# Optimization experiments

Measured on AMD Instinct MI355X. Metric: run time of the kernel, lower is better.

## Reference

```python
import jax, jax.numpy as jnp
import numpy as np

NUM_HEADS = 8
AGENT_NUM = 64
THETA = 0.7


def conv2d(x, w, pad, groups=1):
    return jax.lax.conv_general_dilated(
        x, w, window_strides=(1, 1), padding=[(pad, pad), (pad, pad)],
        dimension_numbers=("NCHW", "OIHW", "NCHW"), feature_group_count=groups)


def setup_inputs() -> dict:
    key = jax.random.key(0)
    ks = jax.random.split(key, 8)
    B, C, H, W = 8, 256, 64, 64
    return {
        "x": jax.random.normal(ks[0], (B, C, H, W), jnp.float32),
        "qkv_w": jax.random.normal(ks[1], (3 * C, C, 3, 3), jnp.float32) * 0.05,
        "qkv_s": 1.0 + 0.05 * jax.random.normal(ks[2], (3 * C,), jnp.float32),
        "qkv_b": 0.05 * jax.random.normal(ks[3], (3 * C,), jnp.float32),
        "pe_w": jax.random.normal(ks[4], (C, 1, 3, 3), jnp.float32) * 0.05,
        "pe_s": 1.0 + 0.05 * jax.random.normal(ks[5], (C,), jnp.float32),
        "pe_b": 0.05 * jax.random.normal(ks[5], (C,), jnp.float32),
        "proj_w": jax.random.normal(ks[6], (C, C, 1, 1), jnp.float32) * 0.05,
        "proj_s": 1.0 + 0.05 * jax.random.normal(ks[7], (C,), jnp.float32),
        "proj_b": 0.05 * jax.random.normal(ks[7], (C,), jnp.float32),
    }


def reference(x, qkv_w, qkv_s, qkv_b, pe_w, pe_s, pe_b, proj_w, proj_s, proj_b):
    B, C, H, W = x.shape
    h, n = NUM_HEADS, AGENT_NUM
    d = C // h
    scale = d ** -0.5
    ps = int(n ** 0.5)  # pool_size = 8

    # Conv_dif (mode='hv'): normal 3x3 conv minus theta * (1x1 conv with hv-summed weights)
    out_n = conv2d(x, qkv_w, pad=1)
    dif_w = qkv_w.reshape(3 * C, C, 9)[:, :, jnp.array([1, 3, 4, 5, 7])].sum(-1)[:, :, None, None]
    out_d = conv2d(x, dif_w, pad=0)
    qkv = (out_n - THETA * out_d) * qkv_s[:, None, None] + qkv_b[:, None, None]  # folded BN

    q, k, v = jnp.split(qkv, 3, axis=1)  # each [B, C, H, W]
    qh = q.reshape(B, h, d, H * W)
    kh = k.reshape(B, h, d, H * W)
    vh = v.reshape(B, h, d, H * W)

    # adaptive avg pool q -> agent tokens (exact block mean since H,W % ps == 0)
    a = q.reshape(B, C, ps, H // ps, ps, W // ps).mean(axis=(3, 5))  # [B, C, ps, ps]
    a = a.reshape(B, C, n).transpose(0, 2, 1).reshape(B, n, h, d).transpose(0, 2, 3, 1)  # [B,h,d,n]

    # stage 1: agents attend to keys, aggregate values
    attn_k = jax.nn.softmax(jnp.einsum("bhdn,bhdN->bhnN", a, kh) * scale, axis=-1)
    attn = jnp.einsum("bhnN,bhdN->bhnd", attn_k, vh)  # [B,h,n,d]

    # stage 2: queries attend to agents
    q_attn = jax.nn.softmax(jnp.einsum("bhdN,bhdn->bhNn", qh, a) * scale, axis=-1)
    out = jnp.einsum("bhNn,bhnd->bhdN", q_attn, attn).reshape(B, C, H, W)

    # depthwise positional encoding on v (BN folded)
    pe = conv2d(v, pe_w, pad=1, groups=C) * pe_s[:, None, None] + pe_b[:, None, None]
    out = out + pe

    # 1x1 projection (BN folded, Identity act)
    out = conv2d(out, proj_w, pad=0) * proj_s[:, None, None] + proj_b[:, None, None]
    return out
```

## Files before the change

### kernel.cpp

```cpp
#include <hip/hip_runtime.h>
#include <cstdint>

typedef __attribute__((ext_vector_type(8))) short short8;
typedef __attribute__((ext_vector_type(4))) float f32x4;

#define THETA 0.7f
#define SCALE 0.17677669529663687f

__device__ __forceinline__ ushort f2b(float f) {
    uint32_t u = __float_as_uint(f);
    u += 0x7FFFu + ((u >> 16) & 1u);
    return (ushort)(u >> 16);
}
__device__ __forceinline__ float b2f(ushort b) {
    return __uint_as_float(((uint32_t)b) << 16);
}

__global__ __launch_bounds__(256) void k_pad(const float* __restrict__ x, ushort* __restrict__ xp) {
    int b = blockIdx.x >> 6, y = blockIdx.x & 63;
    int t = threadIdx.x;
    __shared__ float buf[64][65];
    for (int cc = 0; cc < 4; ++cc) {
        __syncthreads();
#pragma unroll
        for (int i = 0; i < 16; ++i) {
            int idx = i * 256 + t;
            int c = idx >> 6, xx = idx & 63;
            buf[c][xx] = x[(((size_t)b * 256 + cc * 64 + c) << 12) + (y << 6) + xx];
        }
        __syncthreads();
#pragma unroll
        for (int i = 0; i < 16; ++i) {
            int idx = i * 256 + t;
            int xx = idx >> 6, c = idx & 63;
            xp[((size_t)(b * 66 + y + 1) * 66 + (xx + 1)) * 256 + cc * 64 + c] = f2b(buf[c][xx]);
        }
    }
}

__global__ __launch_bounds__(256) void k_foldw(const float* __restrict__ w, const float* __restrict__ s,
                                               ushort* __restrict__ Wa) {
    int o = blockIdx.x, c = threadIdx.x;
    const float* wp = w + ((size_t)o * 256 + c) * 9;
    float v[9];
#pragma unroll
    for (int p = 0; p < 9; ++p) v[p] = wp[p];
    float hv = v[1] + v[3] + v[4] + v[5] + v[7];
    v[4] -= THETA * hv;
    float sc = s[o];
#pragma unroll
    for (int p = 0; p < 9; ++p)
        Wa[(size_t)o * 2304 + p * 256 + c] = f2b(v[p] * sc);
}

__global__ __launch_bounds__(256) void k_foldp(const float* __restrict__ w, const float* __restrict__ s,
                                               ushort* __restrict__ Wh, ushort* __restrict__ Wl) {
    int o = blockIdx.x, c = threadIdx.x;
    float v = w[(size_t)o * 256 + c] * s[o];
    ushort hi = f2b(v);
    Wh[(size_t)o * 256 + c] = hi;
    Wl[(size_t)o * 256 + c] = f2b(v - b2f(hi));
}

__global__ __launch_bounds__(256) void k_conv(const ushort* __restrict__ xp, const ushort* __restrict__ Wa,
                                              const float* __restrict__ qbias, float* __restrict__ qkv) {
    __shared__ ushort Al[128][40];
    __shared__ ushort Bl[128][40];
    const int t = threadIdx.x;
    const int bid0 = blockIdx.x;
    const int bid = (bid0 & 7) * 192 + (bid0 >> 3);
    const int b = bid / 192;
    const int ob = (bid % 192) >> 5;
    const int pb = bid & 31;
    const int o0 = ob << 7;
    const int lane = t & 63;
    const int w = t >> 6;
    const int rw = t >> 2;
    const int q4 = t & 3;
    const ushort* Ag0 = Wa + (size_t)(o0 + rw) * 2304 + q4 * 8;
    const ushort* Ag1 = Ag0 + (size_t)64 * 2304;
    const int y0 = pb * 2;
    const size_t xb = (size_t)b * 66 * 66 * 256;

    f32x4 acc[4][4] = {};

    const int ow2 = (w >> 1) << 6;
    const int pw2 = (w & 1) << 6;
    const int fr = lane & 15;
    const int fs = (lane >> 4) << 3;

    uint4 ra0, ra1, rb0, rb1;
    auto loadk = [&](int kn) {
        int pp = kn >> 3;
        int c0 = (kn & 7) << 5;
        int ky = pp / 3, kx = pp - ky * 3;
        ra0 = *(const uint4*)(Ag0 + kn * 32);
        ra1 = *(const uint4*)(Ag1 + kn * 32);
        const ushort* bp = xp + xb + ((size_t)((y0 + ky) * 66 + (rw + kx))) * 256 + c0 + q4 * 8;
        rb0 = *(const uint4*)bp;
        rb1 = *(const uint4*)(bp + 66 * 256);
    };
    loadk(0);
    for (int kc = 0; kc < 72; ++kc) {
        if (kc) __syncthreads();
        *(uint4*)&Al[rw][q4 * 8] = ra0;
        *(uint4*)&Al[rw + 64][q4 * 8] = ra1;
        *(uint4*)&Bl[rw][q4 * 8] = rb0;
        *(uint4*)&Bl[rw + 64][q4 * 8] = rb1;
        __syncthreads();
        if (kc < 71) loadk(kc + 1);
        short8 af[4], bf[4];
#pragma unroll
        for (int i = 0; i < 4; ++i) af[i] = *(const short8*)&Al[ow2 + i * 16 + fr][fs];
#pragma unroll
        for (int j = 0; j < 4; ++j) bf[j] = *(const short8*)&Bl[pw2 + j * 16 + fr][fs];
#pragma unroll
        for (int i = 0; i < 4; ++i)
#pragma unroll
            for (int j = 0; j < 4; ++j)
                acc[i][j] = __builtin_amdgcn_mfma_f32_16x16x32_bf16(af[i], bf[j], acc[i][j], 0, 0, 0);
    }
    const int pbase = pb * 128 + pw2 + (lane & 15);
#pragma unroll
    for (int i = 0; i < 4; ++i) {
        int o = o0 + ow2 + i * 16 + (lane >> 4) * 4;
#pragma unroll
        for (int r = 0; r < 4; ++r) {
            float bias = qbias[o + r];
            float* dst = qkv + ((size_t)b * 768 + o + r) * 4096 + pbase;
#pragma unroll
            for (int j = 0; j < 4; ++j)
                dst[j * 16] = acc[i][j][r] + bias;
        }
    }
}

__global__ __launch_bounds__(256) void k_pool(const float* __restrict__ qkv, float* __restrict__ ap) {
    const int bid = blockIdx.x;
    const int b = bid >> 8, c = bid & 255;
    const int t = threadIdx.x;
    const int y = t >> 2, xq = t & 3;
    __shared__ float lp[64][8];
    const float* qp = qkv + ((size_t)b * 768 + c) * 4096 + y * 64 + xq * 16;
    f32x4 v0 = *(const f32x4*)(qp);
    f32x4 v1 = *(const f32x4*)(qp + 4);
    f32x4 v2 = *(const f32x4*)(qp + 8);
    f32x4 v3 = *(const f32x4*)(qp + 12);
    lp[y][xq * 2] = v0.x + v0.y + v0.z + v0.w + v1.x + v1.y + v1.z + v1.w;
    lp[y][xq * 2 + 1] = v2.x + v2.y + v2.z + v2.w + v3.x + v3.y + v3.z + v3.w;
    __syncthreads();
    if (t < 64) {
        int py = t >> 3, px = t & 7;
        float s = 0;
#pragma unroll
        for (int r = 0; r < 8; ++r) s += lp[py * 8 + r][px];
        ap[((size_t)b * 256 + c) * 64 + t] = s * (1.0f / 64.0f);
    }
}

__global__ __launch_bounds__(256) void k_att1(const float* __restrict__ qkv, const float* __restrict__ ap,
                                              float* __restrict__ attn_g, float* __restrict__ s_g) {
    const int bid0 = blockIdx.x;
    const int bid = (bid0 & 7) * 64 + (bid0 >> 3);
    const int seg = bid & 7, h = (bid >> 3) & 7, b = bid >> 6;
    const int t = threadIdx.x;
    __shared__ float a_s[64][36];
    __shared__ ushort EL[256][68];
    __shared__ ushort vL[256][40];
#pragma unroll
    for (int i = 0; i < 8; ++i) {
        int idx = i * 256 + t;
        int n = idx & 63, d = idx >> 6;
        a_s[n][d] = ap[((size_t)b * 256 + h * 32 + d) * 64 + n] * SCALE;
    }
    const float* kb = qkv + ((size_t)b * 768 + 256 + h * 32) * 4096;
    const float* vb = qkv + ((size_t)b * 768 + 512 + h * 32) * 4096;
    const int n_own = t >> 2;
    const int dl = t & 3;
    float accr[8] = {0, 0, 0, 0, 0, 0, 0, 0};
    float s_acc = 0.f;
    __syncthreads();
    for (int chunk = 0; chunk < 2; ++chunk) {
        int pix = (seg * 2 + chunk) * 256 + t;
        float kr[32];
#pragma unroll
        for (int d = 0; d < 32; ++d) kr[d] = kb[(size_t)d * 4096 + pix];
#pragma unroll
        for (int i = 0; i < 4; ++i) {
            uint4 pk;
            pk.x = (uint32_t)f2b(vb[(size_t)(8 * i + 0) * 4096 + pix]) |
                   ((uint32_t)f2b(vb[(size_t)(8 * i + 1) * 4096 + pix]) << 16);
            pk.y = (uint32_t)f2b(vb[(size_t)(8 * i + 2) * 4096 + pix]) |
                   ((uint32_t)f2b(vb[(size_t)(8 * i + 3) * 4096 + pix]) << 16);
            pk.z = (uint32_t)f2b(vb[(size_t)(8 * i + 4) * 4096 + pix]) |
                   ((uint32_t)f2b(vb[(size_t)(8 * i + 5) * 4096 + pix]) << 16);
            pk.w = (uint32_t)f2b(vb[(size_t)(8 * i + 6) * 4096 + pix]) |
                   ((uint32_t)f2b(vb[(size_t)(8 * i + 7) * 4096 + pix]) << 16);
            *(uint4*)&vL[t][i * 8] = pk;
        }
#pragma unroll 1
        for (int np = 0; np < 32; ++np) {
            float l0 = 0, l1 = 0;
#pragma unroll
            for (int dq = 0; dq < 8; ++dq) {
                f32x4 a0 = *(const f32x4*)&a_s[2 * np][dq * 4];
                f32x4 a1 = *(const f32x4*)&a_s[2 * np + 1][dq * 4];
                l0 += a0.x * kr[dq * 4] + a0.y * kr[dq * 4 + 1] + a0.z * kr[dq * 4 + 2] + a0.w * kr[dq * 4 + 3];
                l1 += a1.x * kr[dq * 4] + a1.y * kr[dq * 4 + 1] + a1.z * kr[dq * 4 + 2] + a1.w * kr[dq * 4 + 3];
            }
            uint32_t e2 = (uint32_t)f2b(__expf(l0)) | ((uint32_t)f2b(__expf(l1)) << 16);
            *(uint32_t*)&EL[t][2 * np] = e2;
        }
        __syncthreads();
#pragma unroll 1
        for (int tt = 0; tt < 256; ++tt) {
            float e = b2f(EL[tt][n_own]);
            if (dl == 0) s_acc += e;
            ushort4 va = *(const ushort4*)&vL[tt][dl * 8];
            ushort4 vbx = *(const ushort4*)&vL[tt][dl * 8 + 4];
            accr[0] += e * b2f(va.x);
            accr[1] += e * b2f(va.y);
            accr[2] += e * b2f(va.z);
            accr[3] += e * b2f(va.w);
            accr[4] += e * b2f(vbx.x);
            accr[5] += e * b2f(vbx.y);
            accr[6] += e * b2f(vbx.z);
            accr[7] += e * b2f(vbx.w);
        }
        __syncthreads();
    }
#pragma unroll
    for (int i = 0; i < 8; ++i)
        atomicAdd(&attn_g[(((size_t)b * 8 + h) * 64 + n_own) * 32 + dl * 8 + i], accr[i]);
    if (dl == 0) atomicAdd(&s_g[((size_t)b * 8 + h) * 64 + n_own], s_acc);
}

__global__ __launch_bounds__(256) void k_att2(const float* __restrict__ qkv, const float* __restrict__ ap,
                                              const float* __restrict__ attn_g, const float* __restrict__ s_g,
                                              float* __restrict__ outp) {
    const int bid0 = blockIdx.x;
    const int bid = (bid0 & 7) * 128 + (bid0 >> 3);
    const int ch = bid & 15, h = (bid >> 4) & 7, b = bid >> 7;
    const int t = threadIdx.x;
    __shared__ float a2[64][36];
    __shared__ float at2[64][36];
    __shared__ float sInv[64];
#pragma unroll
    for (int i = 0; i < 8; ++i) {
        int idx = i * 256 + t;
        int n = idx & 63, d = idx >> 6;
        a2[n][d] = ap[((size_t)b * 256 + h * 32 + d) * 64 + n] * SCALE;
    }
    if (t < 64) sInv[t] = 1.0f / s_g[((size_t)b * 8 + h) * 64 + t];
    __syncthreads();
#pragma unroll
    for (int i = 0; i < 8; ++i) {
        int idx = i * 256 + t;
        int n = idx >> 5, d = idx & 31;
        at2[n][d] = attn_g[(((size_t)b * 8 + h) * 64 + n) * 32 + d] * sInv[n];
    }
    __syncthreads();
    const float* qb = qkv + ((size_t)b * 768 + h * 32) * 4096;
    int pix = ch * 256 + t;
    float qr[32];
#pragma unroll
    for (int d = 0; d < 32; ++d) qr[d] = qb[(size_t)d * 4096 + pix];
    float oacc[32] = {};
    float s = 0.f;
#pragma unroll 1
    for (int n = 0; n < 64; ++n) {
        float l = 0;
#pragma unroll
        for (int dq = 0; dq < 8; ++dq) {
            f32x4 av = *(const f32x4*)&a2[n][dq * 4];
            l += av.x * qr[dq * 4] + av.y * qr[dq * 4 + 1] + av.z * qr[dq * 4 + 2] + av.w * qr[dq * 4 + 3];
        }
        float e = __expf(l);
        s += e;
#pragma unroll
        for (int dq = 0; dq < 8; ++dq) {
            f32x4 tv = *(const f32x4*)&at2[n][dq * 4];
            oacc[dq * 4] += e * tv.x;
            oacc[dq * 4 + 1] += e * tv.y;
            oacc[dq * 4 + 2] += e * tv.z;
            oacc[dq * 4 + 3] += e * tv.w;
        }
    }
    float si = 1.0f / s;
#pragma unroll
    for (int d = 0; d < 32; ++d)
        outp[((size_t)b * 256 + h * 32 + d) * 4096 + pix] = oacc[d] * si;
}

__global__ __launch_bounds__(256) void k_pe(const float* __restrict__ qkv, const float* __restrict__ pw,
                                            const float* __restrict__ ps, const float* __restrict__ pbias,
                                            float* __restrict__ outp) {
    int gid = blockIdx.x * 256 + threadIdx.x;
    int x4 = (gid & 15) << 2;
    int y = (gid >> 4) & 63;
    int c = (gid >> 10) & 255;
    int b = gid >> 18;
    const float* vp = qkv + ((size_t)b * 768 + 512 + c) * 4096;
    const float* wp = pw + c * 9;
    float s0 = 0, s1 = 0, s2 = 0, s3 = 0;
#pragma unroll
    for (int ky = 0; ky < 3; ++ky) {
        int yy = y + ky - 1;
        if ((unsigned)yy >= 64u) continue;
        const float* rp = vp + yy * 64 + x4;
        f32x4 m = *(const f32x4*)rp;
        float lft = (x4 > 0) ? rp[-1] : 0.f;
        float rgt = (x4 < 60) ? rp[4] : 0.f;
        float w0 = wp[ky * 3], w1 = wp[ky * 3 + 1], w2 = wp[ky * 3 + 2];
        s0 += w0 * lft + w1 * m.x + w2 * m.y;
        s1 += w0 * m.x + w1 * m.y + w2 * m.z;
        s2 += w0 * m.y + w1 * m.z + w2 * m.w;
        s3 += w0 * m.z + w1 * m.w + w2 * rgt;
    }
    float sc = ps[c], bb = pbias[c];
    float* op = outp + ((size_t)b * 256 + c) * 4096 + y * 64 + x4;
    f32x4 o = *(const f32x4*)op;
    o.x += sc * s0 + bb;
    o.y += sc * s1 + bb;
    o.z += sc * s2 + bb;
    o.w += sc * s3 + bb;
    *(f32x4*)op = o;
}

__global__ __launch_bounds__(256) void k_proj(const float* __restrict__ outp, const ushort* __restrict__ Wh,
                                              const ushort* __restrict__ Wl, const float* __restrict__ pbias,
                                              float* __restrict__ out) {
    __shared__ ushort Ah[128][40];
    __shared__ ushort Alo[128][40];
    __shared__ ushort Xl[32][132];
    const int t = threadIdx.x;
    const int bid0 = blockIdx.x;
    const int bid = (bid0 & 7) * 64 + (bid0 >> 3);
    const int b = bid >> 6;
    const int ob = (bid >> 5) & 1;
    const int pb = bid & 31;
    const int o0 = ob << 7;
    const int p0 = pb << 7;
    const int lane = t & 63;
    const int w = t >> 6;
    const int rw = t >> 2, q4 = t & 3;
    const int cl = t >> 3, pg = t & 7;
    const int ow2 = (w >> 1) << 6;
    const int pw2 = (w & 1) << 6;
    const int fr = lane & 15;
    const int fs = (lane >> 4) << 3;

    f32x4 acc[4][4] = {};
    uint4 rah0, rah1, ral0, ral1;
    f32x4 rx[4];
    auto loadk = [&](int kc) {
        const size_t awoff = (size_t)(o0 + rw) * 256 + kc * 32 + q4 * 8;
        rah0 = *(const uint4*)(Wh + awoff);
        rah1 = *(const uint4*)(Wh + awoff + (size_t)64 * 256);
        ral0 = *(const uint4*)(Wl + awoff);
        ral1 = *(const uint4*)(Wl + awoff + (size_t)64 * 256);
        const float* xsrc = outp + ((size_t)b * 256 + kc * 32 + cl) * 4096 + p0 + pg * 16;
#pragma unroll
        for (int m = 0; m < 4; ++m) rx[m] = *(const f32x4*)(xsrc + m * 4);
    };
    loadk(0);
    for (int kc = 0; kc < 8; ++kc) {
        if (kc) __syncthreads();
        *(uint4*)&Ah[rw][q4 * 8] = rah0;
        *(uint4*)&Ah[rw + 64][q4 * 8] = rah1;
        *(uint4*)&Alo[rw][q4 * 8] = ral0;
        *(uint4*)&Alo[rw + 64][q4 * 8] = ral1;
#pragma unroll
        for (int m = 0; m < 4; ++m) {
            ushort4 u;
            u.x = f2b(rx[m].x);
            u.y = f2b(rx[m].y);
            u.z = f2b(rx[m].z);
            u.w = f2b(rx[m].w);
            *(ushort4*)&Xl[cl][pg * 16 + m * 4] = u;
        }
        __syncthreads();
        if (kc < 7) loadk(kc + 1);
        short8 ah[4], al[4], bf[4];
#pragma unroll
        for (int i = 0; i < 4; ++i) {
            ah[i] = *(const short8*)&Ah[ow2 + i * 16 + fr][fs];
            al[i] = *(const short8*)&Alo[ow2 + i * 16 + fr][fs];
        }
#pragma unroll
        for (int j = 0; j < 4; ++j) {
            int pl = pw2 + j * 16 + fr;
#pragma unroll
            for (int kk = 0; kk < 8; ++kk) bf[j][kk] = (short)Xl[fs + kk][pl];
        }
#pragma unroll
        for (int i = 0; i < 4; ++i)
#pragma unroll
            for (int j = 0; j < 4; ++j) {
                acc[i][j] = __builtin_amdgcn_mfma_f32_16x16x32_bf16(ah[i], bf[j], acc[i][j], 0, 0, 0);
                acc[i][j] = __builtin_amdgcn_mfma_f32_16x16x32_bf16(al[i], bf[j], acc[i][j], 0, 0, 0);
            }
    }
    const int pbase = p0 + pw2 + (lane & 15);
#pragma unroll
    for (int i = 0; i < 4; ++i) {
        int o = o0 + ow2 + i * 16 + (lane >> 4) * 4;
#pragma unroll
        for (int r = 0; r < 4; ++r) {
            float bias = pbias[o + r];
            float* dst = out + ((size_t)b * 256 + o + r) * 4096 + pbase;
#pragma unroll
            for (int j = 0; j < 4; ++j)
                dst[j * 16] = acc[i][j][r] + bias;
        }
    }
}

extern "C" void kernel_launch(void* const* d_in, const int* in_sizes, int n_in,
                              void* d_out, int out_size, void* d_ws, size_t ws_size,
                              hipStream_t stream) {
    const float* x = (const float*)d_in[0];
    const float* qkv_w = (const float*)d_in[1];
    const float* qkv_s = (const float*)d_in[2];
    const float* qkv_b = (const float*)d_in[3];
    const float* pe_w = (const float*)d_in[4];
    const float* pe_s = (const float*)d_in[5];
    const float* pe_b = (const float*)d_in[6];
    const float* proj_w = (const float*)d_in[7];
    const float* proj_s = (const float*)d_in[8];
    const float* proj_b = (const float*)d_in[9];
    float* out = (float*)d_out;

    char* ws = (char*)d_ws;
    ushort* xp = (ushort*)(ws);
    ushort* Wa = (ushort*)(ws + 17842176);
    float* qkv = (float*)(ws + 21381120);
    float* apool = (float*)(ws + 122044416);
    float* attn_g = (float*)(ws + 122568704);
    float* s_g = (float*)(ws + 123092992);
    float* outp = (float*)(ws + 123109376);
    ushort* Wh = (ushort*)(ws + 156663808);
    ushort* Wl = (ushort*)(ws + 156794880);

    hipMemsetAsync(xp, 0, 17842176, stream);
    hipMemsetAsync(attn_g, 0, 524288 + 16384, stream);
    k_pad<<<512, 256, 0, stream>>>(x, xp);
    k_foldw<<<768, 256, 0, stream>>>(qkv_w, qkv_s, Wa);
    k_foldp<<<256, 256, 0, stream>>>(proj_w, proj_s, Wh, Wl);
    k_conv<<<1536, 256, 0, stream>>>(xp, Wa, qkv_b, qkv);
    k_pool<<<2048, 256, 0, stream>>>(qkv, apool);
    k_att1<<<512, 256, 0, stream>>>(qkv, apool, attn_g, s_g);
    k_att2<<<1024, 256, 0, stream>>>(qkv, apool, attn_g, s_g, outp);
    k_pe<<<8192, 256, 0, stream>>>(qkv, pe_w, pe_s, pe_b, outp);
    k_proj<<<512, 256, 0, stream>>>(outp, Wh, Wl, proj_b, out);
}
```

Baseline: 451.8 us.

## Store qkv and attention output in bf16 and fuse positional conv into att2

```diff
diff --git a/kernel.cpp b/kernel.cpp
--- a/kernel.cpp
+++ b/kernel.cpp
@@ -63,7 +63,7 @@
 }
 
 __global__ __launch_bounds__(256) void k_conv(const ushort* __restrict__ xp, const ushort* __restrict__ Wa,
-                                              const float* __restrict__ qbias, float* __restrict__ qkv) {
+                                              const float* __restrict__ qbias, ushort* __restrict__ qkv) {
     __shared__ ushort Al[128][40];
     __shared__ ushort Bl[128][40];
     const int t = threadIdx.x;
@@ -127,27 +127,30 @@
 #pragma unroll
         for (int r = 0; r < 4; ++r) {
             float bias = qbias[o + r];
-            float* dst = qkv + ((size_t)b * 768 + o + r) * 4096 + pbase;
+            ushort* dst = qkv + ((size_t)b * 768 + o + r) * 4096 + pbase;
 #pragma unroll
             for (int j = 0; j < 4; ++j)
-                dst[j * 16] = acc[i][j][r] + bias;
-        }
-    }
-}
-
-__global__ __launch_bounds__(256) void k_pool(const float* __restrict__ qkv, float* __restrict__ ap) {
+                dst[j * 16] = f2b(acc[i][j][r] + bias);
+        }
+    }
+}
+
+__global__ __launch_bounds__(256) void k_pool(const ushort* __restrict__ qkv, float* __restrict__ ap) {
     const int bid = blockIdx.x;
     const int b = bid >> 8, c = bid & 255;
     const int t = threadIdx.x;
     const int y = t >> 2, xq = t & 3;
     __shared__ float lp[64][8];
-    const float* qp = qkv + ((size_t)b * 768 + c) * 4096 + y * 64 + xq * 16;
-    f32x4 v0 = *(const f32x4*)(qp);
-    f32x4 v1 = *(const f32x4*)(qp + 4);
-    f32x4 v2 = *(const f32x4*)(qp + 8);
-    f32x4 v3 = *(const f32x4*)(qp + 12);
-    lp[y][xq * 2] = v0.x + v0.y + v0.z + v0.w + v1.x + v1.y + v1.z + v1.w;
-    lp[y][xq * 2 + 1] = v2.x + v2.y + v2.z + v2.w + v3.x + v3.y + v3.z + v3.w;
+    const ushort* qp = qkv + ((size_t)b * 768 + c) * 4096 + y * 64 + xq * 16;
+    short8 a0 = *(const short8*)(qp);
+    short8 a1 = *(const short8*)(qp + 8);
+    float s0 = 0, s1 = 0;
+#pragma unroll
+    for (int j = 0; j < 8; ++j) s0 += b2f((ushort)a0[j]);
+#pragma unroll
+    for (int j = 0; j < 8; ++j) s1 += b2f((ushort)a1[j]);
+    lp[y][xq * 2] = s0;
+    lp[y][xq * 2 + 1] = s1;
     __syncthreads();
     if (t < 64) {
         int py = t >> 3, px = t & 7;
@@ -158,7 +161,7 @@
     }
 }
 
-__global__ __launch_bounds__(256) void k_att1(const float* __restrict__ qkv, const float* __restrict__ ap,
+__global__ __launch_bounds__(256) void k_att1(const ushort* __restrict__ qkv, const float* __restrict__ ap,
                                               float* __restrict__ attn_g, float* __restrict__ s_g) {
     const int bid0 = blockIdx.x;
     const int bid = (bid0 & 7) * 64 + (bid0 >> 3);
@@ -173,8 +176,8 @@
         int n = idx & 63, d = idx >> 6;
         a_s[n][d] = ap[((size_t)b * 256 + h * 32 + d) * 64 + n] * SCALE;
     }
-    const float* kb = qkv + ((size_t)b * 768 + 256 + h * 32) * 4096;
-    const float* vb = qkv + ((size_t)b * 768 + 512 + h * 32) * 4096;
+    const ushort* kb = qkv + ((size_t)b * 768 + 256 + h * 32) * 4096;
+    const ushort* vb = qkv + ((size_t)b * 768 + 512 + h * 32) * 4096;
     const int n_own = t >> 2;
     const int dl = t & 3;
     float accr[8] = {0, 0, 0, 0, 0, 0, 0, 0};
@@ -184,18 +187,18 @@
         int pix = (seg * 2 + chunk) * 256 + t;
         float kr[32];
 #pragma unroll
-        for (int d = 0; d < 32; ++d) kr[d] = kb[(size_t)d * 4096 + pix];
+        for (int d = 0; d < 32; ++d) kr[d] = b2f(kb[(size_t)d * 4096 + pix]);
 #pragma unroll
         for (int i = 0; i < 4; ++i) {
             uint4 pk;
-            pk.x = (uint32_t)f2b(vb[(size_t)(8 * i + 0) * 4096 + pix]) |
-                   ((uint32_t)f2b(vb[(size_t)(8 * i + 1) * 4096 + pix]) << 16);
-            pk.y = (uint32_t)f2b(vb[(size_t)(8 * i + 2) * 4096 + pix]) |
-                   ((uint32_t)f2b(vb[(size_t)(8 * i + 3) * 4096 + pix]) << 16);
-            pk.z = (uint32_t)f2b(vb[(size_t)(8 * i + 4) * 4096 + pix]) |
-                   ((uint32_t)f2b(vb[(size_t)(8 * i + 5) * 4096 + pix]) << 16);
-            pk.w = (uint32_t)f2b(vb[(size_t)(8 * i + 6) * 4096 + pix]) |
-                   ((uint32_t)f2b(vb[(size_t)(8 * i + 7) * 4096 + pix]) << 16);
+            pk.x = (uint32_t)vb[(size_t)(8 * i + 0) * 4096 + pix] |
+                   ((uint32_t)vb[(size_t)(8 * i + 1) * 4096 + pix] << 16);
+            pk.y = (uint32_t)vb[(size_t)(8 * i + 2) * 4096 + pix] |
+                   ((uint32_t)vb[(size_t)(8 * i + 3) * 4096 + pix] << 16);
+            pk.z = (uint32_t)vb[(size_t)(8 * i + 4) * 4096 + pix] |
+                   ((uint32_t)vb[(size_t)(8 * i + 5) * 4096 + pix] << 16);
+            pk.w = (uint32_t)vb[(size_t)(8 * i + 6) * 4096 + pix] |
+                   ((uint32_t)vb[(size_t)(8 * i + 7) * 4096 + pix] << 16);
             *(uint4*)&vL[t][i * 8] = pk;
         }
 #pragma unroll 1
@@ -235,9 +238,10 @@
     if (dl == 0) atomicAdd(&s_g[((size_t)b * 8 + h) * 64 + n_own], s_acc);
 }
 
-__global__ __launch_bounds__(256) void k_att2(const float* __restrict__ qkv, const float* __restrict__ ap,
+__global__ __launch_bounds__(256) void k_att2(const ushort* __restrict__ qkv, const float* __restrict__ ap,
                                               const float* __restrict__ attn_g, const float* __restrict__ s_g,
-                                              float* __restrict__ outp) {
+                                              const float* __restrict__ pe_w, const float* __restrict__ pe_s,
+                                              const float* __restrict__ pe_b, ushort* __restrict__ outp) {
     const int bid0 = blockIdx.x;
     const int bid = (bid0 & 7) * 128 + (bid0 >> 3);
     const int ch = bid & 15, h = (bid >> 4) & 7, b = bid >> 7;
@@ -245,6 +249,9 @@
     __shared__ float a2[64][36];
     __shared__ float at2[64][36];
     __shared__ float sInv[64];
+    __shared__ ushort vsh[32][392];
+    __shared__ float wsh[32][9];
+    __shared__ float psh[32], pbsh[32];
 #pragma unroll
     for (int i = 0; i < 8; ++i) {
         int idx = i * 256 + t;
@@ -252,6 +259,26 @@
         a2[n][d] = ap[((size_t)b * 256 + h * 32 + d) * 64 + n] * SCALE;
     }
     if (t < 64) sInv[t] = 1.0f / s_g[((size_t)b * 8 + h) * 64 + t];
+    if (t < 32) {
+        int c = h * 32 + t;
+#pragma unroll
+        for (int p = 0; p < 9; ++p) wsh[t][p] = pe_w[c * 9 + p];
+        psh[t] = pe_s[c];
+        pbsh[t] = pe_b[c];
+    }
+    {
+        int d = t >> 3, j = t & 7;
+        const ushort* vsrc = qkv + ((size_t)b * 768 + 512 + h * 32 + d) * 4096 + (ch * 4 - 1) * 64;
+        uint4 zz;
+        zz.x = zz.y = zz.z = zz.w = 0u;
+#pragma unroll
+        for (int m = 0; m < 6; ++m) {
+            int e0 = (m * 8 + j) * 8;
+            bool oob = (ch == 0 && e0 < 64) || (ch == 15 && e0 >= 320);
+            uint4 val = oob ? zz : *(const uint4*)(vsrc + e0);
+            *(uint4*)&vsh[d][e0] = val;
+        }
+    }
     __syncthreads();
 #pragma unroll
     for (int i = 0; i < 8; ++i) {
@@ -260,11 +287,11 @@
         at2[n][d] = attn_g[(((size_t)b * 8 + h) * 64 + n) * 32 + d] * sInv[n];
     }
     __syncthreads();
-    const float* qb = qkv + ((size_t)b * 768 + h * 32) * 4096;
+    const ushort* qb = qkv + ((size_t)b * 768 + h * 32) * 4096;
     int pix = ch * 256 + t;
     float qr[32];
 #pragma unroll
-    for (int d = 0; d < 32; ++d) qr[d] = qb[(size_t)d * 4096 + pix];
+    for (int d = 0; d < 32; ++d) qr[d] = b2f(qb[(size_t)d * 4096 + pix]);
     float oacc[32] = {};
     float s = 0.f;
 #pragma unroll 1
@@ -287,47 +314,23 @@
         }
     }
     float si = 1.0f / s;
-#pragma unroll
-    for (int d = 0; d < 32; ++d)
-        outp[((size_t)b * 256 + h * 32 + d) * 4096 + pix] = oacc[d] * si;
-}
-
-__global__ __launch_bounds__(256) void k_pe(const float* __restrict__ qkv, const float* __restrict__ pw,
-                                            const float* __restrict__ ps, const float* __restrict__ pbias,
-                                            float* __restrict__ outp) {
-    int gid = blockIdx.x * 256 + threadIdx.x;
-    int x4 = (gid & 15) << 2;
-    int y = (gid >> 4) & 63;
-    int c = (gid >> 10) & 255;
-    int b = gid >> 18;
-    const float* vp = qkv + ((size_t)b * 768 + 512 + c) * 4096;
-    const float* wp = pw + c * 9;
-    float s0 = 0, s1 = 0, s2 = 0, s3 = 0;
-#pragma unroll
-    for (int ky = 0; ky < 3; ++ky) {
-        int yy = y + ky - 1;
-        if ((unsigned)yy >= 64u) continue;
-        const float* rp = vp + yy * 64 + x4;
-        f32x4 m = *(const f32x4*)rp;
-        float lft = (x4 > 0) ? rp[-1] : 0.f;
-        float rgt = (x4 < 60) ? rp[4] : 0.f;
-        float w0 = wp[ky * 3], w1 = wp[ky * 3 + 1], w2 = wp[ky * 3 + 2];
-        s0 += w0 * lft + w1 * m.x + w2 * m.y;
-        s1 += w0 * m.x + w1 * m.y + w2 * m.z;
-        s2 += w0 * m.y + w1 * m.z + w2 * m.w;
-        s3 += w0 * m.z + w1 * m.w + w2 * rgt;
-    }
-    float sc = ps[c], bb = pbias[c];
-    float* op = outp + ((size_t)b * 256 + c) * 4096 + y * 64 + x4;
-    f32x4 o = *(const f32x4*)op;
-    o.x += sc * s0 + bb;
-    o.y += sc * s1 + bb;
-    o.z += sc * s2 + bb;
-    o.w += sc * s3 + bb;
-    *(f32x4*)op = o;
-}
-
-__global__ __launch_bounds__(256) void k_proj(const float* __restrict__ outp, const ushort* __restrict__ Wh,
+    const int rr = t >> 6, x = t & 63;
+#pragma unroll
+    for (int d = 0; d < 32; ++d) {
+        float pe = 0;
+#pragma unroll
+        for (int ky = 0; ky < 3; ++ky) {
+            int base = (rr + ky) * 64 + x;
+            float mid = b2f(vsh[d][base]);
+            float lft = (x > 0) ? b2f(vsh[d][base - 1]) : 0.f;
+            float rgt = (x < 63) ? b2f(vsh[d][base + 1]) : 0.f;
+            pe += wsh[d][ky * 3] * lft + wsh[d][ky * 3 + 1] * mid + wsh[d][ky * 3 + 2] * rgt;
+        }
+        outp[((size_t)b * 256 + h * 32 + d) * 4096 + pix] = f2b(oacc[d] * si + psh[d] * pe + pbsh[d]);
+    }
+}
+
+__global__ __launch_bounds__(256) void k_proj(const ushort* __restrict__ outp, const ushort* __restrict__ Wh,
                                               const ushort* __restrict__ Wl, const float* __restrict__ pbias,
                                               float* __restrict__ out) {
     __shared__ ushort Ah[128][40];
@@ -351,17 +354,16 @@
     const int fs = (lane >> 4) << 3;
 
     f32x4 acc[4][4] = {};
-    uint4 rah0, rah1, ral0, ral1;
-    f32x4 rx[4];
+    uint4 rah0, rah1, ral0, ral1, rx0, rx1;
     auto loadk = [&](int kc) {
         const size_t awoff = (size_t)(o0 + rw) * 256 + kc * 32 + q4 * 8;
         rah0 = *(const uint4*)(Wh + awoff);
         rah1 = *(const uint4*)(Wh + awoff + (size_t)64 * 256);
         ral0 = *(const uint4*)(Wl + awoff);
         ral1 = *(const uint4*)(Wl + awoff + (size_t)64 * 256);
-        const float* xsrc = outp + ((size_t)b * 256 + kc * 32 + cl) * 4096 + p0 + pg * 16;
-#pragma unroll
-        for (int m = 0; m < 4; ++m) rx[m] = *(const f32x4*)(xsrc + m * 4);
+        const ushort* xsrc = outp + ((size_t)b * 256 + kc * 32 + cl) * 4096 + p0 + pg * 16;
+        rx0 = *(const uint4*)xsrc;
+        rx1 = *(const uint4*)(xsrc + 8);
     };
     loadk(0);
     for (int kc = 0; kc < 8; ++kc) {
@@ -370,15 +372,8 @@
         *(uint4*)&Ah[rw + 64][q4 * 8] = rah1;
         *(uint4*)&Alo[rw][q4 * 8] = ral0;
         *(uint4*)&Alo[rw + 64][q4 * 8] = ral1;
-#pragma unroll
-        for (int m = 0; m < 4; ++m) {
-            ushort4 u;
-            u.x = f2b(rx[m].x);
-            u.y = f2b(rx[m].y);
-            u.z = f2b(rx[m].z);
-            u.w = f2b(rx[m].w);
-            *(ushort4*)&Xl[cl][pg * 16 + m * 4] = u;
-        }
+        *(uint4*)&Xl[cl][pg * 16] = rx0;
+        *(uint4*)&Xl[cl][pg * 16 + 8] = rx1;
         __syncthreads();
         if (kc < 7) loadk(kc + 1);
         short8 ah[4], al[4], bf[4];
@@ -434,23 +429,22 @@
     char* ws = (char*)d_ws;
     ushort* xp = (ushort*)(ws);
     ushort* Wa = (ushort*)(ws + 17842176);
-    float* qkv = (float*)(ws + 21381120);
-    float* apool = (float*)(ws + 122044416);
-    float* attn_g = (float*)(ws + 122568704);
-    float* s_g = (float*)(ws + 123092992);
-    float* outp = (float*)(ws + 123109376);
-    ushort* Wh = (ushort*)(ws + 156663808);
-    ushort* Wl = (ushort*)(ws + 156794880);
+    ushort* qkvb = (ushort*)(ws + 21381120);
+    float* apool = (float*)(ws + 71712768);
+    float* attn_g = (float*)(ws + 72237056);
+    float* s_g = (float*)(ws + 72761344);
+    ushort* outpb = (ushort*)(ws + 72777728);
+    ushort* Wh = (ushort*)(ws + 89554944);
+    ushort* Wl = (ushort*)(ws + 89686016);
 
     hipMemsetAsync(xp, 0, 17842176, stream);
     hipMemsetAsync(attn_g, 0, 524288 + 16384, stream);
     k_pad<<<512, 256, 0, stream>>>(x, xp);
     k_foldw<<<768, 256, 0, stream>>>(qkv_w, qkv_s, Wa);
     k_foldp<<<256, 256, 0, stream>>>(proj_w, proj_s, Wh, Wl);
-    k_conv<<<1536, 256, 0, stream>>>(xp, Wa, qkv_b, qkv);
-    k_pool<<<2048, 256, 0, stream>>>(qkv, apool);
-    k_att1<<<512, 256, 0, stream>>>(qkv, apool, attn_g, s_g);
-    k_att2<<<1024, 256, 0, stream>>>(qkv, apool, attn_g, s_g, outp);
-    k_pe<<<8192, 256, 0, stream>>>(qkv, pe_w, pe_s, pe_b, outp);
-    k_proj<<<512, 256, 0, stream>>>(outp, Wh, Wl, proj_b, out);
-}
+    k_conv<<<1536, 256, 0, stream>>>(xp, Wa, qkv_b, qkvb);
+    k_pool<<<2048, 256, 0, stream>>>(qkvb, apool);
+    k_att1<<<512, 256, 0, stream>>>(qkvb, apool, attn_g, s_g);
+    k_att2<<<1024, 256, 0, stream>>>(qkvb, apool, attn_g, s_g, pe_w, pe_s, pe_b, outpb);
+    k_proj<<<512, 256, 0, stream>>>(outpb, Wh, Wl, proj_b, out);
+}
```

Measured after the change: 432.2 us. -4.3%, faster.
